# Performance work log

Hardware: AMD Instinct MI355X
Metric: run time of the kernel (lower is better)

The kernel has to match this reference:

```python
import jax, jax.numpy as jnp
import numpy as np

S, B, D, H, DFF = 1024, 4, 1024, 16, 4096
HD = D // H
EPS = 1e-5


def setup_inputs() -> dict:
    key = jax.random.key(0)
    ks = jax.random.split(key, 16)

    def w(k, shape):
        return jax.random.normal(k, shape, jnp.float32) * 0.02

    inp = {
        "input": jax.random.normal(ks[0], (S, B, D), jnp.float32),  # [seq, batch, d_model]
        "enc": jax.random.normal(ks[1], (S, B, D), jnp.float32),
    }
    i = 2
    for pfx in ("sa", "ca"):
        for name in ("wq", "wk", "wv", "wo"):
            inp[f"{pfx}_{name}"] = w(ks[i], (D, D)); i += 1
            inp[f"{pfx}_b{name[1]}"] = jnp.zeros((D,), jnp.float32)
    inp["w1"] = w(ks[i], (DFF, D)); i += 1
    inp["b1"] = jnp.zeros((DFF,), jnp.float32)
    inp["w2"] = w(ks[i], (D, DFF)); i += 1
    inp["b2"] = jnp.zeros((D,), jnp.float32)
    for n in (1, 2, 3):
        inp[f"ln{n}_g"] = jnp.ones((D,), jnp.float32)
        inp[f"ln{n}_b"] = jnp.zeros((D,), jnp.float32)
    return inp


def _layernorm(x, g, b):
    m = x.mean(-1, keepdims=True)
    v = x.var(-1, keepdims=True)
    return (x - m) * jax.lax.rsqrt(v + EPS) * g + b


def _mha(query, key, value, wq, bq, wk, bk, wv, bv, wo, bo):
    # query/key/value: [seq, batch, d_model] (seq-first layout)
    def proj(x, w, b):
        y = x @ w.T + b
        s, bsz, _ = y.shape
        return y.reshape(s, bsz, H, HD)  # [s, b, h, hd]

    q = proj(query, wq, bq)
    k = proj(key, wk, bk)
    v = proj(value, wv, bv)
    scores = jnp.einsum("sbhd,tbhd->bhst", q, k) / (HD ** 0.5)  # [b, h, s_q, s_k]
    p = jax.nn.softmax(scores, axis=-1)
    o = jnp.einsum("bhst,tbhd->sbhd", p, v)  # [s_q, b, h, hd]
    o = o.reshape(o.shape[0], o.shape[1], D)  # heads concatenated along features
    return o @ wo.T + bo  # [s_q, b, d_model]


def reference(input, enc,
              sa_wq, sa_bq, sa_wk, sa_bk, sa_wv, sa_bv, sa_wo, sa_bo,
              ca_wq, ca_bq, ca_wk, ca_bk, ca_wv, ca_bv, ca_wo, ca_bo,
              w1, b1, w2, b2,
              ln1_g, ln1_b, ln2_g, ln2_b, ln3_g, ln3_b):
    # self-attention: attn_in_1(input, input, input) -> q=k=v=input
    out1 = _mha(input, input, input, sa_wq, sa_bq, sa_wk, sa_bk, sa_wv, sa_bv, sa_wo, sa_bo)
    out = _layernorm(input + out1, ln1_g, ln1_b)
    # cross-attention: attn_in_2(out, enc, enc) binds key=out, query=enc, value=enc
    out2 = _mha(enc, out, enc, ca_wq, ca_bq, ca_wk, ca_bk, ca_wv, ca_bv, ca_wo, ca_bo)
    out = _layernorm(out + out2, ln2_g, ln2_b)
    # FFN (dropout is identity at p=0 / eval)
    out3 = jax.nn.relu(out @ w1.T + b1) @ w2.T + b2
    return _layernorm(out + out3, ln3_g, ln3_b)
```

## Files before the change

### kernel.cpp

```cpp
#include <hip/hip_runtime.h>
#include <hip/hip_bf16.h>
#include <cstdint>
#include <cstddef>


typedef __bf16 bf16;
typedef __attribute__((ext_vector_type(8))) __bf16 bf16x8;
typedef __attribute__((ext_vector_type(4))) __bf16 bf16x4;
typedef __attribute__((ext_vector_type(4))) float f32x4;

#define SEQ   1024
#define BATCH 4
#define DMOD  1024
#define NHEAD 16
#define HDIM  64
#define NTOK  (SEQ*BATCH)
#define DFF   4096

#define GLD(gp, lp) __builtin_amdgcn_global_load_lds( \
    (__attribute__((address_space(1))) void*)(gp),    \
    (__attribute__((address_space(3))) void*)(lp), 16, 0, 0)

struct CastSeg { const float* src; bf16* dst; int n4; };
struct CastArgs { CastSeg seg[12]; };

__global__ __launch_bounds__(256) void cast_multi(CastArgs a) {
  CastSeg s = a.seg[blockIdx.y];
  int i = blockIdx.x * 256 + threadIdx.x;
  if (i < s.n4) {
    float4 v = ((const float4*)s.src)[i];
    bf16x4 o; o[0] = (bf16)v.x; o[1] = (bf16)v.y; o[2] = (bf16)v.z; o[3] = (bf16)v.w;
    ((bf16x4*)s.dst)[i] = o;
  }
}

__global__ __launch_bounds__(256) void gemm_nt(
    const bf16* __restrict__ A, const bf16* __restrict__ W,
    const float* __restrict__ b0, const float* __restrict__ b1,
    const float* __restrict__ b2, const float* __restrict__ b3,
    void* __restrict__ C, int M, int N, int K, int flags, int kc)
{
  __shared__ bf16 As[4096];
  __shared__ bf16 Bs[4096];
  const int tid  = threadIdx.x;
  const int wave = tid >> 6, lane = tid & 63;
  const int quad = lane >> 4, l16 = lane & 15;

  const int nbx = gridDim.x, nby = gridDim.y, nbz = gridDim.z;
  const int lin = blockIdx.x + nbx * (blockIdx.y + nby * blockIdx.z);
  const int c = lin & 7;
  int q = lin >> 3;
  const int bx = q % nbx; q /= nbx;
  const int bz = q % nbz; q /= nbz;
  const int by = c * (nby >> 3) + q;

  const int m0 = by * 128, n0 = bx * 128;
  const int wm = (wave >> 1) * 64, wn = (wave & 1) * 64;

  f32x4 acc[4][4] = {};

  const int srow = tid >> 2;
  const int scol = ((tid & 3) ^ ((srow >> 1) & 3)) * 8;
  const int kbeg = bz * kc;
  const bf16* Ap = A + (size_t)(m0 + srow) * K + scol + kbeg;
  const bf16* Wp = W + (size_t)(n0 + srow) * K + scol + kbeg;
  const size_t rstep = (size_t)64 * K;
  bf16* AsW = As + wave * 512;
  bf16* BsW = Bs + wave * 512;

  const int swz = (l16 >> 1) & 3;
  const int aq = (quad ^ swz) * 8;

  for (int k0 = 0; k0 < kc; k0 += 32) {
    __syncthreads();
    GLD(Ap + k0,         AsW);
    GLD(Ap + rstep + k0, AsW + 2048);
    GLD(Wp + k0,         BsW);
    GLD(Wp + rstep + k0, BsW + 2048);
    __syncthreads();
    bf16x8 wf[4], tf[4];
#pragma unroll
    for (int i = 0; i < 4; ++i)
      wf[i] = *(const bf16x8*)(Bs + (wn + i * 16 + l16) * 32 + aq);
#pragma unroll
    for (int i = 0; i < 4; ++i)
      tf[i] = *(const bf16x8*)(As + (wm + i * 16 + l16) * 32 + aq);
#pragma unroll
    for (int mi = 0; mi < 4; ++mi)
#pragma unroll
      for (int ni = 0; ni < 4; ++ni)
        acc[mi][ni] = __builtin_amdgcn_mfma_f32_16x16x32_bf16(wf[mi], tf[ni], acc[mi][ni], 0, 0, 0);
  }

  if (gridDim.z > 1) {
    float* Cp = (float*)C + (size_t)bz * M * N;
#pragma unroll
    for (int ni = 0; ni < 4; ++ni) {
      const size_t rowb = (size_t)(m0 + wm + ni * 16 + l16) * N;
#pragma unroll
      for (int mi = 0; mi < 4; ++mi) {
        const int gf = n0 + wn + mi * 16 + quad * 4;
        *(f32x4*)(Cp + rowb + gf) = acc[mi][ni];
      }
    }
    return;
  }

  const float* bp[4] = {b0, b1, b2, b3};
  const bool obf = flags & 1, orelu = flags & 2, oscale = flags & 4;
#pragma unroll
  for (int ni = 0; ni < 4; ++ni) {
    const size_t rowb = (size_t)(m0 + wm + ni * 16 + l16) * N;
#pragma unroll
    for (int mi = 0; mi < 4; ++mi) {
      const int gf = n0 + wn + mi * 16 + quad * 4;
      const float4 bi = *(const float4*)(bp[gf >> 10] + (gf & 1023));
      const float sc = (oscale && gf < 1024) ? 0.125f : 1.0f;
      float v0 = (acc[mi][ni][0] + bi.x) * sc;
      float v1 = (acc[mi][ni][1] + bi.y) * sc;
      float v2 = (acc[mi][ni][2] + bi.z) * sc;
      float v3 = (acc[mi][ni][3] + bi.w) * sc;
      if (orelu) {
        v0 = fmaxf(v0, 0.f); v1 = fmaxf(v1, 0.f);
        v2 = fmaxf(v2, 0.f); v3 = fmaxf(v3, 0.f);
      }
      if (obf) {
        bf16x4 o; o[0] = (bf16)v0; o[1] = (bf16)v1; o[2] = (bf16)v2; o[3] = (bf16)v3;
        *(bf16x4*)((bf16*)C + rowb + gf) = o;
      } else {
        float4 o; o.x = v0; o.y = v1; o.z = v2; o.w = v3;
        *(float4*)((float*)C + rowb + gf) = o;
      }
    }
  }
}

__global__ __launch_bounds__(256) void vtrans(
    const bf16* __restrict__ V, int ldv, bf16* __restrict__ VT)
{
  const int tid = threadIdx.x, w = tid >> 6, lane = tid & 63;
  const int b = blockIdx.y >> 4;
  const int co = (blockIdx.y & 15) * HDIM;
  const int s0 = blockIdx.x * 64;
  const int hd0 = blockIdx.z * 32 + w * 8;
  bf16x8 v = *(const bf16x8*)(V + ((size_t)(s0 + lane) * BATCH + b) * ldv + co + hd0);
  const size_t obase = ((size_t)blockIdx.y * HDIM + hd0) * SEQ + s0 + lane;
#pragma unroll
  for (int j = 0; j < 8; ++j)
    VT[obase + (size_t)j * SEQ] = v[j];
}

__global__ __launch_bounds__(256) void attn_kernel(
    const bf16* __restrict__ Q, int ldq,
    const bf16* __restrict__ K, int ldk,
    const bf16* __restrict__ VT,
    bf16* __restrict__ O)
{
  __shared__ bf16 Kt[64 * 64];
  __shared__ bf16 Vt[64 * 64];

  const int tid = threadIdx.x, w = tid >> 6, lane = tid & 63;
  const int quad = lane >> 4, l16 = lane & 15;
  const int bh = blockIdx.y, b = bh >> 4;
  const int co = (bh & 15) * HDIM;
  const int sq0 = blockIdx.x * 128 + w * 32;

  bf16x8 qf[2][2];
#pragma unroll
  for (int u = 0; u < 2; ++u) {
    const bf16* qp = Q + ((size_t)(sq0 + u * 16 + l16) * BATCH + b) * ldq + co + quad * 8;
    qf[u][0] = *(const bf16x8*)qp;
    qf[u][1] = *(const bf16x8*)(qp + 32);
  }

  f32x4 oacc[2][4] = {};
  float lsum[2] = {0.f, 0.f};

  const int srow = lane >> 3;
  const int glog = (lane & 7) ^ srow;
  const int sw = l16 & 7;

  for (int t0 = 0; t0 < SEQ; t0 += 64) {
    __syncthreads();
#pragma unroll
    for (int j = 0; j < 2; ++j) {
      const int slot = j * 32 + w * 8 + srow;
      const int m = slot & 15, half = (slot >> 4) & 1, chunk = slot >> 5;
      const int t = chunk * 32 + 8 * (m >> 2) + 4 * half + (m & 3);
      GLD(K + ((size_t)(t0 + t) * BATCH + b) * ldk + co + glog * 8,
          Kt + (j * 32 + w * 8) * 64);
      const int hd = j * 32 + w * 8 + srow;
      GLD(VT + ((size_t)bh * HDIM + hd) * SEQ + t0 + glog * 8,
          Vt + (j * 32 + w * 8) * 64);
    }
    __syncthreads();

#pragma unroll
    for (int c = 0; c < 2; ++c) {
      const bf16* k0 = Kt + (c * 32 + l16) * 64;
      const bf16* k1 = Kt + (c * 32 + 16 + l16) * 64;
      const int g0 = (quad ^ sw) * 8;
      const int g1 = ((4 + quad) ^ sw) * 8;
      bf16x8 ka00 = *(const bf16x8*)(k0 + g0);
      bf16x8 ka01 = *(const bf16x8*)(k0 + g1);
      bf16x8 ka10 = *(const bf16x8*)(k1 + g0);
      bf16x8 ka11 = *(const bf16x8*)(k1 + g1);
      bf16x8 vf[4];
#pragma unroll
      for (int nt = 0; nt < 4; ++nt)
        vf[nt] = *(const bf16x8*)(Vt + (nt * 16 + l16) * 64 + (((c * 4 + quad) ^ sw) * 8));
#pragma unroll
      for (int u = 0; u < 2; ++u) {
        f32x4 c0 = {}, c1 = {};
        c0 = __builtin_amdgcn_mfma_f32_16x16x32_bf16(ka00, qf[u][0], c0, 0, 0, 0);
        c0 = __builtin_amdgcn_mfma_f32_16x16x32_bf16(ka01, qf[u][1], c0, 0, 0, 0);
        c1 = __builtin_amdgcn_mfma_f32_16x16x32_bf16(ka10, qf[u][0], c1, 0, 0, 0);
        c1 = __builtin_amdgcn_mfma_f32_16x16x32_bf16(ka11, qf[u][1], c1, 0, 0, 0);
        bf16x8 pf; float ls = 0.f;
#pragma unroll
        for (int r = 0; r < 4; ++r) {
          float p0 = __expf(c0[r]);
          float p1 = __expf(c1[r]);
          ls += p0 + p1;
          pf[r] = (bf16)p0;
          pf[4 + r] = (bf16)p1;
        }
        lsum[u] += ls;
#pragma unroll
        for (int nt = 0; nt < 4; ++nt)
          oacc[u][nt] = __builtin_amdgcn_mfma_f32_16x16x32_bf16(pf, vf[nt], oacc[u][nt], 0, 0, 0);
      }
    }
  }

#pragma unroll
  for (int u = 0; u < 2; ++u) {
    float s = lsum[u];
    s += __shfl_xor(s, 16, 64);
    s += __shfl_xor(s, 32, 64);
#pragma unroll
    for (int r = 0; r < 4; ++r) {
      const float inv = 1.0f / __shfl(s, quad * 4 + r, 64);
      const size_t ro = ((size_t)(sq0 + u * 16 + quad * 4 + r) * BATCH + b) * DMOD + co;
#pragma unroll
      for (int nt = 0; nt < 4; ++nt)
        O[ro + nt * 16 + l16] = (bf16)(oacc[u][nt][r] * inv);
    }
  }
}

__global__ __launch_bounds__(256) void add_ln_red(
    const float* __restrict__ Xa,
    const float* __restrict__ p0, const float* __restrict__ p1,
    const float* __restrict__ p2, const float* __restrict__ p3, int np,
    const float* __restrict__ bias,
    const float* __restrict__ g, const float* __restrict__ beta,
    float* __restrict__ outf, bf16* __restrict__ outb)
{
  const int row = blockIdx.x, tid = threadIdx.x;
  const size_t base = (size_t)row * DMOD;
  float4 a = ((const float4*)(Xa + base))[tid];
  float4 q0 = ((const float4*)(p0 + base))[tid];
  float4 q1 = ((const float4*)(p1 + base))[tid];
  float x0 = a.x + q0.x + q1.x, x1 = a.y + q0.y + q1.y;
  float x2 = a.z + q0.z + q1.z, x3 = a.w + q0.w + q1.w;
  if (np > 2) {
    float4 q2 = ((const float4*)(p2 + base))[tid];
    float4 q3 = ((const float4*)(p3 + base))[tid];
    x0 += q2.x + q3.x; x1 += q2.y + q3.y; x2 += q2.z + q3.z; x3 += q2.w + q3.w;
  }
  float4 bi = ((const float4*)bias)[tid];
  x0 += bi.x; x1 += bi.y; x2 += bi.z; x3 += bi.w;

  float s  = x0 + x1 + x2 + x3;
  float s2 = x0 * x0 + x1 * x1 + x2 * x2 + x3 * x3;
#pragma unroll
  for (int m = 1; m < 64; m <<= 1) { s += __shfl_xor(s, m, 64); s2 += __shfl_xor(s2, m, 64); }
  __shared__ float red[8];
  if ((tid & 63) == 0) { red[tid >> 6] = s; red[4 + (tid >> 6)] = s2; }
  __syncthreads();
  s  = red[0] + red[1] + red[2] + red[3];
  s2 = red[4] + red[5] + red[6] + red[7];
  const float mean = s * (1.0f / DMOD);
  const float var  = s2 * (1.0f / DMOD) - mean * mean;
  const float rs   = rsqrtf(var + 1e-5f);
  float4 gv = ((const float4*)g)[tid];
  float4 bv = ((const float4*)beta)[tid];
  float y0 = (x0 - mean) * rs * gv.x + bv.x;
  float y1 = (x1 - mean) * rs * gv.y + bv.y;
  float y2 = (x2 - mean) * rs * gv.z + bv.z;
  float y3 = (x3 - mean) * rs * gv.w + bv.w;
  float4 o; o.x = y0; o.y = y1; o.z = y2; o.w = y3;
  ((float4*)(outf + base))[tid] = o;
  if (outb) {
    bf16x4 ob; ob[0] = (bf16)y0; ob[1] = (bf16)y1; ob[2] = (bf16)y2; ob[3] = (bf16)y3;
    ((bf16x4*)(outb + base))[tid] = ob;
  }
}

__global__ __launch_bounds__(256) void reduce_cast(
    const float* __restrict__ p0, const float* __restrict__ p1,
    const float* __restrict__ bias, bf16* __restrict__ out)
{
  const int row = blockIdx.x, tid = threadIdx.x;
  const size_t base = (size_t)row * DMOD;
  float4 a = ((const float4*)(p0 + base))[tid];
  float4 b = ((const float4*)(p1 + base))[tid];
  float4 bi = ((const float4*)bias)[tid];
  bf16x4 o;
  o[0] = (bf16)(a.x + b.x + bi.x); o[1] = (bf16)(a.y + b.y + bi.y);
  o[2] = (bf16)(a.z + b.z + bi.z); o[3] = (bf16)(a.w + b.w + bi.w);
  ((bf16x4*)(out + base))[tid] = o;
}

extern "C" void kernel_launch(void* const* d_in, const int* in_sizes, int n_in,
                              void* d_out, int out_size, void* d_ws, size_t ws_size,
                              hipStream_t stream)
{
  const float* x0    = (const float*)d_in[0];
  const float* enc   = (const float*)d_in[1];
  const float* sa_wq = (const float*)d_in[2];
  const float* sa_bq = (const float*)d_in[3];
  const float* sa_wk = (const float*)d_in[4];
  const float* sa_bk = (const float*)d_in[5];
  const float* sa_wv = (const float*)d_in[6];
  const float* sa_bv = (const float*)d_in[7];
  const float* sa_wo = (const float*)d_in[8];
  const float* sa_bo = (const float*)d_in[9];
  const float* ca_wq = (const float*)d_in[10];
  const float* ca_bq = (const float*)d_in[11];
  const float* ca_wk = (const float*)d_in[12];
  const float* ca_bk = (const float*)d_in[13];
  const float* ca_wv = (const float*)d_in[14];
  const float* ca_bv = (const float*)d_in[15];
  const float* ca_wo = (const float*)d_in[16];
  const float* ca_bo = (const float*)d_in[17];
  const float* w1    = (const float*)d_in[18];
  const float* b1    = (const float*)d_in[19];
  const float* w2    = (const float*)d_in[20];
  const float* b2    = (const float*)d_in[21];
  const float* ln1g  = (const float*)d_in[22];
  const float* ln1b  = (const float*)d_in[23];
  const float* ln2g  = (const float*)d_in[24];
  const float* ln2b  = (const float*)d_in[25];
  const float* ln3g  = (const float*)d_in[26];
  const float* ln3b  = (const float*)d_in[27];

  char* ws = (char*)d_ws;
  size_t off = 0;
  auto take = [&](size_t bytes) -> char* {
    char* p = ws + off; off += (bytes + 255) & ~(size_t)255; return p;
  };
  const size_t WEL = (size_t)DMOD * DMOD;
  const size_t ACT = (size_t)NTOK * DMOD;
  bf16*  Wqkv_s = (bf16*)take(3 * WEL * 2);
  bf16*  Wo_s   = (bf16*)take(WEL * 2);
  bf16*  Wqv_c  = (bf16*)take(2 * WEL * 2);
  bf16*  Wk_c   = (bf16*)take(WEL * 2);
  bf16*  Wo_c   = (bf16*)take(WEL * 2);
  bf16*  W1b    = (bf16*)take(4 * WEL * 2);
  bf16*  W2b    = (bf16*)take(4 * WEL * 2);
  char*  regP   = take(32 * 1024 * 1024);
  bf16*  x0b    = (bf16*)regP;
  bf16*  QKVs   = (bf16*)(regP + 8 * 1024 * 1024);
  float* part0  = (float*)regP;
  float* part1  = (float*)(regP + 16 * 1024 * 1024);
  bf16*  QVc    = (bf16*)regP;
  bf16*  Kc     = (bf16*)(regP + 16 * 1024 * 1024);
  char*  regE   = take(16 * 1024 * 1024);
  bf16*  encb   = (bf16*)regE;
  bf16*  ctx    = (bf16*)(regE + 8 * 1024 * 1024);
  float* part3  = (float*)regE;
  float* out1f  = (float*)take(ACT * 4);
  float* part2  = out1f;
  bf16*  out1b  = (bf16*)take(ACT * 2);
  float* out2f  = (float*)take(ACT * 4);
  bf16*  out2b  = (bf16*)take(ACT * 2);
  char*  regH   = take((size_t)NTOK * DFF * 2);
  bf16*  Hff    = (bf16*)regH;
  float* wkp0   = (float*)regH;
  float* wkp1   = (float*)(regH + 16 * 1024 * 1024);
  bf16*  VT     = (bf16*)take(ACT * 2);
  (void)ws_size; (void)in_sizes; (void)n_in; (void)out_size;

  CastArgs cargs;
  const int nw  = (int)(WEL / 4);
  const int ntk = (int)(ACT / 4);
  cargs.seg[0]  = {x0,    x0b,            ntk};
  cargs.seg[1]  = {enc,   encb,           ntk};
  cargs.seg[2]  = {sa_wq, Wqkv_s,         nw};
  cargs.seg[3]  = {sa_wk, Wqkv_s + WEL,   nw};
  cargs.seg[4]  = {sa_wv, Wqkv_s + 2*WEL, nw};
  cargs.seg[5]  = {sa_wo, Wo_s,           nw};
  cargs.seg[6]  = {ca_wq, Wqv_c,          nw};
  cargs.seg[7]  = {ca_wv, Wqv_c + WEL,    nw};
  cargs.seg[8]  = {ca_wk, Wk_c,           nw};
  cargs.seg[9]  = {ca_wo, Wo_c,           nw};
  cargs.seg[10] = {w1,    W1b,            nw * 4};
  cargs.seg[11] = {w2,    W2b,            nw * 4};
  cast_multi<<<dim3((ntk + 255) / 256, 12), 256, 0, stream>>>(cargs);

  auto gemm = [&](const bf16* A, const bf16* Wt,
                  const float* bb0, const float* bb1, const float* bb2, const float* bb3,
                  void* Cp, int M, int N, int Kd, int flags, int nz) {
    gemm_nt<<<dim3(N / 128, M / 128, nz), 256, 0, stream>>>(
        A, Wt, bb0, bb1, bb2, bb3, Cp, M, N, Kd, flags, Kd / nz);
  };

  gemm(x0b, Wqkv_s, sa_bq, sa_bk, sa_bv, sa_bv, QKVs, NTOK, 3 * DMOD, DMOD, 1 | 4, 1);
  vtrans<<<dim3(SEQ / 64, BATCH * NHEAD, 2), 256, 0, stream>>>(QKVs + 2 * DMOD, 3 * DMOD, VT);
  attn_kernel<<<dim3(SEQ / 128, BATCH * NHEAD), 256, 0, stream>>>(
      QKVs, 3 * DMOD, QKVs + DMOD, 3 * DMOD, VT, ctx);
  gemm(ctx, Wo_s, nullptr, nullptr, nullptr, nullptr, part0, NTOK, DMOD, DMOD, 0, 2);
  add_ln_red<<<dim3(NTOK), 256, 0, stream>>>(x0, part0, part1, nullptr, nullptr, 2,
                                             sa_bo, ln1g, ln1b, out1f, out1b);
  gemm(encb, Wqv_c, ca_bq, ca_bv, ca_bv, ca_bv, QVc, NTOK, 2 * DMOD, DMOD, 1 | 4, 1);
  gemm(out1b, Wk_c, nullptr, nullptr, nullptr, nullptr, wkp0, NTOK, DMOD, DMOD, 0, 2);
  reduce_cast<<<dim3(NTOK), 256, 0, stream>>>(wkp0, wkp1, ca_bk, Kc);
  vtrans<<<dim3(SEQ / 64, BATCH * NHEAD, 2), 256, 0, stream>>>(QVc + DMOD, 2 * DMOD, VT);
  attn_kernel<<<dim3(SEQ / 128, BATCH * NHEAD), 256, 0, stream>>>(
      QVc, 2 * DMOD, Kc, DMOD, VT, ctx);
  gemm(ctx, Wo_c, nullptr, nullptr, nullptr, nullptr, part0, NTOK, DMOD, DMOD, 0, 2);
  add_ln_red<<<dim3(NTOK), 256, 0, stream>>>(out1f, part0, part1, nullptr, nullptr, 2,
                                             ca_bo, ln2g, ln2b, out2f, out2b);
  gemm(out2b, W1b, b1, b1 + 1024, b1 + 2048, b1 + 3072, Hff, NTOK, DFF, DMOD, 1 | 2, 1);
  gemm(Hff, W2b, nullptr, nullptr, nullptr, nullptr, part0, NTOK, DMOD, DFF, 0, 4);
  add_ln_red<<<dim3(NTOK), 256, 0, stream>>>(out2f, part0, part1, part2, part3, 4,
                                             b2, ln3g, ln3b, (float*)d_out, nullptr);
}
```

Baseline: 559.0 us.

## Fuse self/cross QKV projections with V-transpose epilogue, BK=64 tiles, bf16 split-K partials

Replaces the separate self-attention QKV GEMM, cross-attention QV GEMM and two vtrans kernels with one gemm_qkv launch whose epilogue writes Q (pre-scaled), K and transposed V directly. The GEMM K-step grows from 32 to 64 with a new swizzled LDS layout, halving barriers per K. Split-K partials are now stored as bf16 instead of fp32, cutting partial-sum traffic but adding rounding error before the residual and layernorm. Buffers are reorganized so the layernorm outputs are written in place.

```diff
diff --git a/kernel.cpp b/kernel.cpp
--- a/kernel.cpp
+++ b/kernel.cpp
@@ -34,14 +34,15 @@
   }
 }
 
+
 __global__ __launch_bounds__(256) void gemm_nt(
     const bf16* __restrict__ A, const bf16* __restrict__ W,
     const float* __restrict__ b0, const float* __restrict__ b1,
     const float* __restrict__ b2, const float* __restrict__ b3,
-    void* __restrict__ C, int M, int N, int K, int flags, int kc)
+    bf16* __restrict__ C, int M, int N, int K, int flags, int kc)
 {
-  __shared__ bf16 As[4096];
-  __shared__ bf16 Bs[4096];
+  __shared__ bf16 As[128 * 64];
+  __shared__ bf16 Bs[128 * 64];
   const int tid  = threadIdx.x;
   const int wave = tid >> 6, lane = tid & 63;
   const int quad = lane >> 4, l16 = lane & 15;
@@ -59,55 +60,60 @@
 
   f32x4 acc[4][4] = {};
 
-  const int srow = tid >> 2;
-  const int scol = ((tid & 3) ^ ((srow >> 1) & 3)) * 8;
+  const int srow8 = lane >> 3;
+  const int sg = ((lane & 7) ^ srow8) * 8;
   const int kbeg = bz * kc;
-  const bf16* Ap = A + (size_t)(m0 + srow) * K + scol + kbeg;
-  const bf16* Wp = W + (size_t)(n0 + srow) * K + scol + kbeg;
-  const size_t rstep = (size_t)64 * K;
-  bf16* AsW = As + wave * 512;
-  bf16* BsW = Bs + wave * 512;
-
-  const int swz = (l16 >> 1) & 3;
-  const int aq = (quad ^ swz) * 8;
-
-  for (int k0 = 0; k0 < kc; k0 += 32) {
+  const bf16* Ap = A + (size_t)(m0 + wave * 32 + srow8) * K + kbeg + sg;
+  const bf16* Wp = W + (size_t)(n0 + wave * 32 + srow8) * K + kbeg + sg;
+  const size_t rstep8 = (size_t)8 * K;
+  bf16* AsW = As + (wave * 32) * 64;
+  bf16* BsW = Bs + (wave * 32) * 64;
+  const int fsw = l16 & 7;
+
+  for (int k0 = 0; k0 < kc; k0 += 64) {
     __syncthreads();
-    GLD(Ap + k0,         AsW);
-    GLD(Ap + rstep + k0, AsW + 2048);
-    GLD(Wp + k0,         BsW);
-    GLD(Wp + rstep + k0, BsW + 2048);
+#pragma unroll
+    for (int j = 0; j < 4; ++j) {
+      GLD(Ap + j * rstep8 + k0, AsW + j * 8 * 64);
+      GLD(Wp + j * rstep8 + k0, BsW + j * 8 * 64);
+    }
     __syncthreads();
-    bf16x8 wf[4], tf[4];
-#pragma unroll
-    for (int i = 0; i < 4; ++i)
-      wf[i] = *(const bf16x8*)(Bs + (wn + i * 16 + l16) * 32 + aq);
-#pragma unroll
-    for (int i = 0; i < 4; ++i)
-      tf[i] = *(const bf16x8*)(As + (wm + i * 16 + l16) * 32 + aq);
-#pragma unroll
-    for (int mi = 0; mi < 4; ++mi)
-#pragma unroll
-      for (int ni = 0; ni < 4; ++ni)
-        acc[mi][ni] = __builtin_amdgcn_mfma_f32_16x16x32_bf16(wf[mi], tf[ni], acc[mi][ni], 0, 0, 0);
-  }
-
-  if (gridDim.z > 1) {
-    float* Cp = (float*)C + (size_t)bz * M * N;
+#pragma unroll
+    for (int ks = 0; ks < 2; ++ks) {
+      const int g = ((ks * 4 + quad) ^ fsw) * 8;
+      bf16x8 wf[4], tf[4];
+#pragma unroll
+      for (int i = 0; i < 4; ++i)
+        wf[i] = *(const bf16x8*)(Bs + (wn + i * 16 + l16) * 64 + g);
+#pragma unroll
+      for (int i = 0; i < 4; ++i)
+        tf[i] = *(const bf16x8*)(As + (wm + i * 16 + l16) * 64 + g);
+#pragma unroll
+      for (int mi = 0; mi < 4; ++mi)
+#pragma unroll
+        for (int ni = 0; ni < 4; ++ni)
+          acc[mi][ni] = __builtin_amdgcn_mfma_f32_16x16x32_bf16(wf[mi], tf[ni], acc[mi][ni], 0, 0, 0);
+    }
+  }
+
+  if (nbz > 1) {
+    bf16* Cp = C + (size_t)bz * M * N;
 #pragma unroll
     for (int ni = 0; ni < 4; ++ni) {
       const size_t rowb = (size_t)(m0 + wm + ni * 16 + l16) * N;
 #pragma unroll
       for (int mi = 0; mi < 4; ++mi) {
         const int gf = n0 + wn + mi * 16 + quad * 4;
-        *(f32x4*)(Cp + rowb + gf) = acc[mi][ni];
+        bf16x4 o; o[0] = (bf16)acc[mi][ni][0]; o[1] = (bf16)acc[mi][ni][1];
+        o[2] = (bf16)acc[mi][ni][2]; o[3] = (bf16)acc[mi][ni][3];
+        *(bf16x4*)(Cp + rowb + gf) = o;
       }
     }
     return;
   }
 
   const float* bp[4] = {b0, b1, b2, b3};
-  const bool obf = flags & 1, orelu = flags & 2, oscale = flags & 4;
+  const bool orelu = flags & 1;
 #pragma unroll
   for (int ni = 0; ni < 4; ++ni) {
     const size_t rowb = (size_t)(m0 + wm + ni * 16 + l16) * N;
@@ -115,46 +121,131 @@
     for (int mi = 0; mi < 4; ++mi) {
       const int gf = n0 + wn + mi * 16 + quad * 4;
       const float4 bi = *(const float4*)(bp[gf >> 10] + (gf & 1023));
-      const float sc = (oscale && gf < 1024) ? 0.125f : 1.0f;
-      float v0 = (acc[mi][ni][0] + bi.x) * sc;
-      float v1 = (acc[mi][ni][1] + bi.y) * sc;
-      float v2 = (acc[mi][ni][2] + bi.z) * sc;
-      float v3 = (acc[mi][ni][3] + bi.w) * sc;
+      float v0 = acc[mi][ni][0] + bi.x, v1 = acc[mi][ni][1] + bi.y;
+      float v2 = acc[mi][ni][2] + bi.z, v3 = acc[mi][ni][3] + bi.w;
       if (orelu) {
         v0 = fmaxf(v0, 0.f); v1 = fmaxf(v1, 0.f);
         v2 = fmaxf(v2, 0.f); v3 = fmaxf(v3, 0.f);
       }
-      if (obf) {
-        bf16x4 o; o[0] = (bf16)v0; o[1] = (bf16)v1; o[2] = (bf16)v2; o[3] = (bf16)v3;
-        *(bf16x4*)((bf16*)C + rowb + gf) = o;
+      bf16x4 o; o[0] = (bf16)v0; o[1] = (bf16)v1; o[2] = (bf16)v2; o[3] = (bf16)v3;
+      *(bf16x4*)(C + rowb + gf) = o;
+    }
+  }
+}
+
+__global__ __launch_bounds__(256) void gemm_qkv(
+    const bf16* __restrict__ x0b, const bf16* __restrict__ encb,
+    const bf16* __restrict__ Wqkv, const bf16* __restrict__ Wqv,
+    const float* __restrict__ sbq, const float* __restrict__ sbk,
+    const float* __restrict__ sbv,
+    const float* __restrict__ cbq, const float* __restrict__ cbv,
+    bf16* __restrict__ Qs, bf16* __restrict__ Ks, bf16* __restrict__ VTs,
+    bf16* __restrict__ Qc, bf16* __restrict__ VTc)
+{
+  __shared__ bf16 As[128 * 64];
+  __shared__ bf16 Bs[128 * 64];
+  const int tid  = threadIdx.x;
+  const int wave = tid >> 6, lane = tid & 63;
+  const int quad = lane >> 4, l16 = lane & 15;
+
+  int id = blockIdx.x, seg, bx, by;
+  const bf16 *A, *W;
+  if (id < 768) {
+    seg = 0; const int c = id & 7, q = id >> 3;
+    by = c * 4 + q / 24; bx = q % 24; A = x0b; W = Wqkv;
+  } else {
+    id -= 768;
+    seg = 1; const int c = id & 7, q = id >> 3;
+    by = c * 4 + q / 16; bx = q % 16; A = encb; W = Wqv;
+  }
+  const int K = 1024;
+  const int m0 = by * 128, n0 = bx * 128;
+  const int wm = (wave >> 1) * 64, wn = (wave & 1) * 64;
+
+  f32x4 acc[4][4] = {};
+  const int srow8 = lane >> 3;
+  const int sg = ((lane & 7) ^ srow8) * 8;
+  const bf16* Ap = A + (size_t)(m0 + wave * 32 + srow8) * K + sg;
+  const bf16* Wp = W + (size_t)(n0 + wave * 32 + srow8) * K + sg;
+  const size_t rstep8 = (size_t)8 * K;
+  bf16* AsW = As + (wave * 32) * 64;
+  bf16* BsW = Bs + (wave * 32) * 64;
+  const int fsw = l16 & 7;
+
+  for (int k0 = 0; k0 < K; k0 += 64) {
+    __syncthreads();
+#pragma unroll
+    for (int j = 0; j < 4; ++j) {
+      GLD(Ap + j * rstep8 + k0, AsW + j * 8 * 64);
+      GLD(Wp + j * rstep8 + k0, BsW + j * 8 * 64);
+    }
+    __syncthreads();
+#pragma unroll
+    for (int ks = 0; ks < 2; ++ks) {
+      const int g = ((ks * 4 + quad) ^ fsw) * 8;
+      bf16x8 wf[4], tf[4];
+#pragma unroll
+      for (int i = 0; i < 4; ++i)
+        wf[i] = *(const bf16x8*)(Bs + (wn + i * 16 + l16) * 64 + g);
+#pragma unroll
+      for (int i = 0; i < 4; ++i)
+        tf[i] = *(const bf16x8*)(As + (wm + i * 16 + l16) * 64 + g);
+#pragma unroll
+      for (int mi = 0; mi < 4; ++mi)
+#pragma unroll
+        for (int ni = 0; ni < 4; ++ni)
+          acc[mi][ni] = __builtin_amdgcn_mfma_f32_16x16x32_bf16(wf[mi], tf[ni], acc[mi][ni], 0, 0, 0);
+    }
+  }
+
+  const int region = n0 >> 10;
+  const bool isV = (seg == 0) ? (region == 2) : (region == 1);
+#pragma unroll
+  for (int ni = 0; ni < 4; ++ni) {
+    const int i = m0 + wm + ni * 16 + l16;
+#pragma unroll
+    for (int mi = 0; mi < 4; ++mi) {
+      const int gf = n0 + wn + mi * 16 + quad * 4;
+      const int lf = gf & 1023;
+      if (!isV) {
+        if (region == 0) {
+          const float* bq = (seg == 0) ? sbq : cbq;
+          const float4 bi = *(const float4*)(bq + lf);
+          bf16* dst = ((seg == 0) ? Qs : Qc) + (size_t)i * 1024 + lf;
+          bf16x4 o;
+          o[0] = (bf16)((acc[mi][ni][0] + bi.x) * 0.125f);
+          o[1] = (bf16)((acc[mi][ni][1] + bi.y) * 0.125f);
+          o[2] = (bf16)((acc[mi][ni][2] + bi.z) * 0.125f);
+          o[3] = (bf16)((acc[mi][ni][3] + bi.w) * 0.125f);
+          *(bf16x4*)dst = o;
+        } else {
+          const float4 bi = *(const float4*)(sbk + lf);
+          bf16x4 o;
+          o[0] = (bf16)(acc[mi][ni][0] + bi.x);
+          o[1] = (bf16)(acc[mi][ni][1] + bi.y);
+          o[2] = (bf16)(acc[mi][ni][2] + bi.z);
+          o[3] = (bf16)(acc[mi][ni][3] + bi.w);
+          *(bf16x4*)(Ks + (size_t)i * 1024 + lf) = o;
+        }
       } else {
-        float4 o; o.x = v0; o.y = v1; o.z = v2; o.w = v3;
-        *(float4*)((float*)C + rowb + gf) = o;
+        const float* bv = (seg == 0) ? sbv : cbv;
+        const float4 bi = *(const float4*)(bv + lf);
+        const int h = lf >> 6, hd = lf & 63;
+        const int b = i & 3, s = i >> 2;
+        bf16* dst = ((seg == 0) ? VTs : VTc)
+                    + (((size_t)b * 16 + h) * 64 + hd) * 1024 + s;
+        dst[0]    = (bf16)(acc[mi][ni][0] + bi.x);
+        dst[1024] = (bf16)(acc[mi][ni][1] + bi.y);
+        dst[2048] = (bf16)(acc[mi][ni][2] + bi.z);
+        dst[3072] = (bf16)(acc[mi][ni][3] + bi.w);
       }
     }
   }
 }
 
-__global__ __launch_bounds__(256) void vtrans(
-    const bf16* __restrict__ V, int ldv, bf16* __restrict__ VT)
-{
-  const int tid = threadIdx.x, w = tid >> 6, lane = tid & 63;
-  const int b = blockIdx.y >> 4;
-  const int co = (blockIdx.y & 15) * HDIM;
-  const int s0 = blockIdx.x * 64;
-  const int hd0 = blockIdx.z * 32 + w * 8;
-  bf16x8 v = *(const bf16x8*)(V + ((size_t)(s0 + lane) * BATCH + b) * ldv + co + hd0);
-  const size_t obase = ((size_t)blockIdx.y * HDIM + hd0) * SEQ + s0 + lane;
-#pragma unroll
-  for (int j = 0; j < 8; ++j)
-    VT[obase + (size_t)j * SEQ] = v[j];
-}
-
 __global__ __launch_bounds__(256) void attn_kernel(
-    const bf16* __restrict__ Q, int ldq,
-    const bf16* __restrict__ K, int ldk,
-    const bf16* __restrict__ VT,
-    bf16* __restrict__ O)
+    const bf16* __restrict__ Q, const bf16* __restrict__ K,
+    const bf16* __restrict__ VT, bf16* __restrict__ O)
 {
   __shared__ bf16 Kt[64 * 64];
   __shared__ bf16 Vt[64 * 64];
@@ -168,7 +259,7 @@
   bf16x8 qf[2][2];
 #pragma unroll
   for (int u = 0; u < 2; ++u) {
-    const bf16* qp = Q + ((size_t)(sq0 + u * 16 + l16) * BATCH + b) * ldq + co + quad * 8;
+    const bf16* qp = Q + ((size_t)(sq0 + u * 16 + l16) * BATCH + b) * 1024 + co + quad * 8;
     qf[u][0] = *(const bf16x8*)qp;
     qf[u][1] = *(const bf16x8*)(qp + 32);
   }
@@ -187,7 +278,7 @@
       const int slot = j * 32 + w * 8 + srow;
       const int m = slot & 15, half = (slot >> 4) & 1, chunk = slot >> 5;
       const int t = chunk * 32 + 8 * (m >> 2) + 4 * half + (m & 3);
-      GLD(K + ((size_t)(t0 + t) * BATCH + b) * ldk + co + glog * 8,
+      GLD(K + ((size_t)(t0 + t) * BATCH + b) * 1024 + co + glog * 8,
           Kt + (j * 32 + w * 8) * 64);
       const int hd = j * 32 + w * 8 + srow;
       GLD(VT + ((size_t)bh * HDIM + hd) * SEQ + t0 + glog * 8,
@@ -251,8 +342,8 @@
 
 __global__ __launch_bounds__(256) void add_ln_red(
     const float* __restrict__ Xa,
-    const float* __restrict__ p0, const float* __restrict__ p1,
-    const float* __restrict__ p2, const float* __restrict__ p3, int np,
+    const bf16* __restrict__ p0, const bf16* __restrict__ p1,
+    const bf16* __restrict__ p2, const bf16* __restrict__ p3, int np,
     const float* __restrict__ bias,
     const float* __restrict__ g, const float* __restrict__ beta,
     float* __restrict__ outf, bf16* __restrict__ outb)
@@ -260,14 +351,17 @@
   const int row = blockIdx.x, tid = threadIdx.x;
   const size_t base = (size_t)row * DMOD;
   float4 a = ((const float4*)(Xa + base))[tid];
-  float4 q0 = ((const float4*)(p0 + base))[tid];
-  float4 q1 = ((const float4*)(p1 + base))[tid];
-  float x0 = a.x + q0.x + q1.x, x1 = a.y + q0.y + q1.y;
-  float x2 = a.z + q0.z + q1.z, x3 = a.w + q0.w + q1.w;
+  bf16x4 q0 = ((const bf16x4*)(p0 + base))[tid];
+  bf16x4 q1 = ((const bf16x4*)(p1 + base))[tid];
+  float x0 = a.x + (float)q0[0] + (float)q1[0];
+  float x1 = a.y + (float)q0[1] + (float)q1[1];
+  float x2 = a.z + (float)q0[2] + (float)q1[2];
+  float x3 = a.w + (float)q0[3] + (float)q1[3];
   if (np > 2) {
-    float4 q2 = ((const float4*)(p2 + base))[tid];
-    float4 q3 = ((const float4*)(p3 + base))[tid];
-    x0 += q2.x + q3.x; x1 += q2.y + q3.y; x2 += q2.z + q3.z; x3 += q2.w + q3.w;
+    bf16x4 q2 = ((const bf16x4*)(p2 + base))[tid];
+    bf16x4 q3 = ((const bf16x4*)(p3 + base))[tid];
+    x0 += (float)q2[0] + (float)q3[0]; x1 += (float)q2[1] + (float)q3[1];
+    x2 += (float)q2[2] + (float)q3[2]; x3 += (float)q2[3] + (float)q3[3];
   }
   float4 bi = ((const float4*)bias)[tid];
   x0 += bi.x; x1 += bi.y; x2 += bi.z; x3 += bi.w;
@@ -299,17 +393,19 @@
 }
 
 __global__ __launch_bounds__(256) void reduce_cast(
-    const float* __restrict__ p0, const float* __restrict__ p1,
+    const bf16* __restrict__ p0, const bf16* __restrict__ p1,
     const float* __restrict__ bias, bf16* __restrict__ out)
 {
   const int row = blockIdx.x, tid = threadIdx.x;
   const size_t base = (size_t)row * DMOD;
-  float4 a = ((const float4*)(p0 + base))[tid];
-  float4 b = ((const float4*)(p1 + base))[tid];
+  bf16x4 a = ((const bf16x4*)(p0 + base))[tid];
+  bf16x4 b = ((const bf16x4*)(p1 + base))[tid];
   float4 bi = ((const float4*)bias)[tid];
   bf16x4 o;
-  o[0] = (bf16)(a.x + b.x + bi.x); o[1] = (bf16)(a.y + b.y + bi.y);
-  o[2] = (bf16)(a.z + b.z + bi.z); o[3] = (bf16)(a.w + b.w + bi.w);
+  o[0] = (bf16)((float)a[0] + (float)b[0] + bi.x);
+  o[1] = (bf16)((float)a[1] + (float)b[1] + bi.y);
+  o[2] = (bf16)((float)a[2] + (float)b[2] + bi.z);
+  o[3] = (bf16)((float)a[3] + (float)b[3] + bi.w);
   ((bf16x4*)(out + base))[tid] = o;
 }
 
@@ -353,34 +449,28 @@
   };
   const size_t WEL = (size_t)DMOD * DMOD;
   const size_t ACT = (size_t)NTOK * DMOD;
-  bf16*  Wqkv_s = (bf16*)take(3 * WEL * 2);
-  bf16*  Wo_s   = (bf16*)take(WEL * 2);
-  bf16*  Wqv_c  = (bf16*)take(2 * WEL * 2);
-  bf16*  Wk_c   = (bf16*)take(WEL * 2);
-  bf16*  Wo_c   = (bf16*)take(WEL * 2);
-  bf16*  W1b    = (bf16*)take(4 * WEL * 2);
-  bf16*  W2b    = (bf16*)take(4 * WEL * 2);
-  char*  regP   = take(32 * 1024 * 1024);
-  bf16*  x0b    = (bf16*)regP;
-  bf16*  QKVs   = (bf16*)(regP + 8 * 1024 * 1024);
-  float* part0  = (float*)regP;
-  float* part1  = (float*)(regP + 16 * 1024 * 1024);
-  bf16*  QVc    = (bf16*)regP;
-  bf16*  Kc     = (bf16*)(regP + 16 * 1024 * 1024);
-  char*  regE   = take(16 * 1024 * 1024);
-  bf16*  encb   = (bf16*)regE;
-  bf16*  ctx    = (bf16*)(regE + 8 * 1024 * 1024);
-  float* part3  = (float*)regE;
-  float* out1f  = (float*)take(ACT * 4);
-  float* part2  = out1f;
-  bf16*  out1b  = (bf16*)take(ACT * 2);
-  float* out2f  = (float*)take(ACT * 4);
-  bf16*  out2b  = (bf16*)take(ACT * 2);
-  char*  regH   = take((size_t)NTOK * DFF * 2);
-  bf16*  Hff    = (bf16*)regH;
-  float* wkp0   = (float*)regH;
-  float* wkp1   = (float*)(regH + 16 * 1024 * 1024);
-  bf16*  VT     = (bf16*)take(ACT * 2);
+  bf16* Wqkv_s = (bf16*)take(3 * WEL * 2);
+  bf16* Wo_s   = (bf16*)take(WEL * 2);
+  bf16* Wqv_c  = (bf16*)take(2 * WEL * 2);
+  bf16* Wk_c   = (bf16*)take(WEL * 2);
+  bf16* Wo_c   = (bf16*)take(WEL * 2);
+  bf16* W1b    = (bf16*)take(4 * WEL * 2);
+  bf16* W2b    = (bf16*)take(4 * WEL * 2);
+  bf16* x0b  = (bf16*)take(ACT * 2);
+  bf16* encb = (bf16*)take(ACT * 2);
+  bf16* Qs   = (bf16*)take(ACT * 2);
+  bf16* Ks   = (bf16*)take(ACT * 2);
+  bf16* VTs  = (bf16*)take(ACT * 2);
+  bf16* Qc   = (bf16*)take(ACT * 2);
+  bf16* VTc  = (bf16*)take(ACT * 2);
+  bf16* Kc   = (bf16*)take(ACT * 2);
+  bf16* ctx  = (bf16*)take(ACT * 2);
+  float* out1f = (float*)take(ACT * 4);
+  bf16*  out1b = (bf16*)take(ACT * 2);
+  bf16*  Hff   = (bf16*)take((size_t)NTOK * DFF * 2);
+  bf16* pA = x0b;  bf16* pB = encb;
+  bf16* pC = Qs;   bf16* pD = Ks;
+  bf16* f0 = Qs;   bf16* f1 = Ks;  bf16* f2 = VTs;  bf16* f3 = Qc;
   (void)ws_size; (void)in_sizes; (void)n_in; (void)out_size;
 
   CastArgs cargs;
@@ -402,29 +492,26 @@
 
   auto gemm = [&](const bf16* A, const bf16* Wt,
                   const float* bb0, const float* bb1, const float* bb2, const float* bb3,
-                  void* Cp, int M, int N, int Kd, int flags, int nz) {
+                  bf16* Cp, int M, int N, int Kd, int flags, int nz) {
     gemm_nt<<<dim3(N / 128, M / 128, nz), 256, 0, stream>>>(
         A, Wt, bb0, bb1, bb2, bb3, Cp, M, N, Kd, flags, Kd / nz);
   };
 
-  gemm(x0b, Wqkv_s, sa_bq, sa_bk, sa_bv, sa_bv, QKVs, NTOK, 3 * DMOD, DMOD, 1 | 4, 1);
-  vtrans<<<dim3(SEQ / 64, BATCH * NHEAD, 2), 256, 0, stream>>>(QKVs + 2 * DMOD, 3 * DMOD, VT);
-  attn_kernel<<<dim3(SEQ / 128, BATCH * NHEAD), 256, 0, stream>>>(
-      QKVs, 3 * DMOD, QKVs + DMOD, 3 * DMOD, VT, ctx);
-  gemm(ctx, Wo_s, nullptr, nullptr, nullptr, nullptr, part0, NTOK, DMOD, DMOD, 0, 2);
-  add_ln_red<<<dim3(NTOK), 256, 0, stream>>>(x0, part0, part1, nullptr, nullptr, 2,
+  gemm_qkv<<<dim3(1280), 256, 0, stream>>>(
+      x0b, encb, Wqkv_s, Wqv_c, sa_bq, sa_bk, sa_bv, ca_bq, ca_bv,
+      Qs, Ks, VTs, Qc, VTc);
+  attn_kernel<<<dim3(SEQ / 128, BATCH * NHEAD), 256, 0, stream>>>(Qs, Ks, VTs, ctx);
+  gemm(ctx, Wo_s, nullptr, nullptr, nullptr, nullptr, pA, NTOK, DMOD, DMOD, 0, 2);
+  add_ln_red<<<dim3(NTOK), 256, 0, stream>>>(x0, pA, pB, nullptr, nullptr, 2,
                                              sa_bo, ln1g, ln1b, out1f, out1b);
-  gemm(encb, Wqv_c, ca_bq, ca_bv, ca_bv, ca_bv, QVc, NTOK, 2 * DMOD, DMOD, 1 | 4, 1);
-  gemm(out1b, Wk_c, nullptr, nullptr, nullptr, nullptr, wkp0, NTOK, DMOD, DMOD, 0, 2);
-  reduce_cast<<<dim3(NTOK), 256, 0, stream>>>(wkp0, wkp1, ca_bk, Kc);
-  vtrans<<<dim3(SEQ / 64, BATCH * NHEAD, 2), 256, 0, stream>>>(QVc + DMOD, 2 * DMOD, VT);
-  attn_kernel<<<dim3(SEQ / 128, BATCH * NHEAD), 256, 0, stream>>>(
-      QVc, 2 * DMOD, Kc, DMOD, VT, ctx);
-  gemm(ctx, Wo_c, nullptr, nullptr, nullptr, nullptr, part0, NTOK, DMOD, DMOD, 0, 2);
-  add_ln_red<<<dim3(NTOK), 256, 0, stream>>>(out1f, part0, part1, nullptr, nullptr, 2,
-                                             ca_bo, ln2g, ln2b, out2f, out2b);
-  gemm(out2b, W1b, b1, b1 + 1024, b1 + 2048, b1 + 3072, Hff, NTOK, DFF, DMOD, 1 | 2, 1);
-  gemm(Hff, W2b, nullptr, nullptr, nullptr, nullptr, part0, NTOK, DMOD, DFF, 0, 4);
-  add_ln_red<<<dim3(NTOK), 256, 0, stream>>>(out2f, part0, part1, part2, part3, 4,
+  gemm(out1b, Wk_c, nullptr, nullptr, nullptr, nullptr, pC, NTOK, DMOD, DMOD, 0, 2);
+  reduce_cast<<<dim3(NTOK), 256, 0, stream>>>(pC, pD, ca_bk, Kc);
+  attn_kernel<<<dim3(SEQ / 128, BATCH * NHEAD), 256, 0, stream>>>(Qc, Kc, VTc, ctx);
+  gemm(ctx, Wo_c, nullptr, nullptr, nullptr, nullptr, pA, NTOK, DMOD, DMOD, 0, 2);
+  add_ln_red<<<dim3(NTOK), 256, 0, stream>>>(out1f, pA, pB, nullptr, nullptr, 2,
+                                             ca_bo, ln2g, ln2b, out1f, out1b);
+  gemm(out1b, W1b, b1, b1 + 1024, b1 + 2048, b1 + 3072, Hff, NTOK, DFF, DMOD, 1, 1);
+  gemm(Hff, W2b, nullptr, nullptr, nullptr, nullptr, f0, NTOK, DMOD, DFF, 0, 4);
+  add_ln_red<<<dim3(NTOK), 256, 0, stream>>>(out1f, f0, f1, f2, f3, 4,
                                              b2, ln3g, ln3b, (float*)d_out, nullptr);
 }
```

New measurement: 512.1 us. -8.4%, faster.
